# Performance work log

Hardware: AMD Instinct MI355X
Metric: run time of the kernel (lower is better)

Reference implementation:

```python
import jax, jax.numpy as jnp
import numpy as np

B, T, K = 512, 512, 128


def setup_inputs() -> dict:
    key = jax.random.key(0)
    k1, k2, k3, k4, k5 = jax.random.split(key, 5)
    emissions = jax.random.normal(k1, (B, T, K), dtype=jnp.float32)
    tags = jax.random.randint(k2, (B, T), 0, K, dtype=jnp.int64)
    mask = jnp.ones((B, T), dtype=jnp.bool_)
    # learned CRF params, init uniform(-0.1, 0.1) as in reset_parameters
    transitions = jax.random.uniform(k3, (K, K), jnp.float32, -0.1, 0.1)
    start_transitions = jax.random.uniform(k4, (K,), jnp.float32, -0.1, 0.1)
    end_transitions = jax.random.uniform(k5, (K,), jnp.float32, -0.1, 0.1)
    return {
        "emissions": emissions,
        "tags": tags,
        "mask": mask,
        "transitions": transitions,
        "start_transitions": start_transitions,
        "end_transitions": end_transitions,
    }


def _log_partition(emissions, mask, transitions, start_transitions, end_transitions):
    # emissions: [T, B, K] time-major; mask: [T, B]
    log_alpha0 = start_transitions[None, :] + emissions[0]  # [B, K]

    def step(log_alpha, inp):
        em_t, m_t = inp  # [B, K], [B]
        # inner[b, i, j] = log_alpha[b, i] + transitions[i, j] + em_t[b, j]
        inner = log_alpha[:, :, None] + transitions[None, :, :] + em_t[:, None, :]
        new = jax.nn.logsumexp(inner, axis=1)  # [B, K]
        log_alpha = jnp.where(m_t[:, None], new, log_alpha)
        return log_alpha, None

    log_alpha, _ = jax.lax.scan(step, log_alpha0, (emissions[1:], mask[1:]))
    log_alpha = log_alpha + end_transitions[None, :]
    return jax.nn.logsumexp(log_alpha, axis=1)  # [B]


def _gold_score(emissions, tags, mask, transitions, start_transitions, end_transitions):
    # time-major emissions [T, B, K], tags/mask [T, B]
    maskf = mask.astype(emissions.dtype)
    score = start_transitions[tags[0]]  # [B]
    # emission scores: gather tag emission at each step, masked
    em = jnp.take_along_axis(emissions, tags[:, :, None], axis=2)[:, :, 0]  # [T, B]
    score = score + jnp.sum(em * maskf, axis=0)
    # transition scores: transitions[tags[i], tags[i-1]] (note [to, from] order, as in source)
    trans = transitions[tags[1:], tags[:-1]]  # [T-1, B]
    score = score + jnp.sum(trans * maskf[1:], axis=0)
    last_idx = jnp.sum(mask.astype(jnp.int32), axis=0) - 1  # [B]
    last_tags = jnp.take_along_axis(tags, last_idx[None, :], axis=0)[0]  # [B]
    score = score + end_transitions[last_tags]
    return score


def reference(emissions, tags, mask, transitions, start_transitions, end_transitions):
    # batch_first=True -> transpose to time-major
    em = jnp.transpose(emissions, (1, 0, 2))  # [T, B, K]
    tg = jnp.transpose(tags, (1, 0))  # [T, B]
    mk = jnp.transpose(mask, (1, 0))  # [T, B]
    log_num = _gold_score(em, tg, mk, transitions, start_transitions, end_transitions)
    log_den = _log_partition(em, mk, transitions, start_transitions, end_transitions)
    return -jnp.mean(log_num - log_den)
```

## Files before the change

### kernel.cpp

```cpp
#include <hip/hip_runtime.h>

#define K 128
#define T 512
#define BB 512
#define PADB 20

typedef float f32x2 __attribute__((ext_vector_type(2)));
typedef float f32x4 __attribute__((ext_vector_type(4)));

#define LDS_BARRIER() asm volatile("s_waitcnt lgkmcnt(0)\ns_barrier" ::: "memory")

template <int CTRL>
__device__ __forceinline__ float qperm(float x) {
    return __int_as_float(__builtin_amdgcn_update_dpp(
        0, __float_as_int(x), CTRL, 0xF, 0xF, true));
}
#define QXOR1   0xB1
#define QXOR2   0x4E
#define HMIRROR 0x141

__global__ __launch_bounds__(512, 4) void mega_kernel(
    const float* __restrict__ em, const int* __restrict__ tags,
    const float* __restrict__ trans, const float* __restrict__ startt,
    const float* __restrict__ endt,
    float* __restrict__ log_den, float* __restrict__ log_num)
{
    const int bid  = blockIdx.x;
    const int kind = (bid ^ (bid >> 8)) & 1;
    const int b    = bid >> 1;
    const int tid  = threadIdx.x;

    __shared__ __align__(16) float stF[2][8 * PADB];
    __shared__ __align__(16) float stB[2][8 * PADB];
    __shared__ float gs[8];
    __shared__ int   iks[2];

    if (kind) {
        const int* tg = tags + (size_t)b * T;
        const float* emb = em + (size_t)b * T * K;
        int   tag = tg[tid];
        float s   = emb[(size_t)tid * K + tag];
        if (tid >= 1) s += trans[tag * K + tg[tid - 1]];
#pragma unroll
        for (int off = 32; off >= 1; off >>= 1) s += __shfl_xor(s, off);
        if ((tid & 63) == 0) gs[tid >> 6] = s;
        __syncthreads();
        if (tid == 0) {
            float tot = ((gs[0] + gs[1]) + (gs[2] + gs[3]))
                      + ((gs[4] + gs[5]) + (gs[6] + gs[7]));
            log_num[b] = tot + startt[tg[0]] + endt[tg[T - 1]];
        }
        return;
    }

    const int half = tid >> 8;
    const int h    = tid & 255;
    const int ib   = h & 7;
    const int jg   = h >> 3;
    const int own  = 4 * jg + (ib & 3);
    const bool writer = (ib < 4);
    const int wpos = (own >> 4) * PADB + (own & 15);

    f32x2 Ec[32];
    {
        const volatile float* Tv = trans;
        const int r0 = ib * 16, c0 = jg * 4;
#pragma unroll
        for (int c = 0; c < 4; ++c)
#pragma unroll
            for (int p = 0; p < 8; ++p) {
                float x0, x1;
                if (half == 0) {
                    x0 = Tv[(size_t)(r0 + 2 * p)     * K + c0 + c];
                    x1 = Tv[(size_t)(r0 + 2 * p + 1) * K + c0 + c];
                } else {
                    x0 = Tv[(size_t)(c0 + c) * K + r0 + 2 * p];
                    x1 = Tv[(size_t)(c0 + c) * K + r0 + 2 * p + 1];
                }
                Ec[c * 8 + p].x = __expf(x0);
                Ec[c * 8 + p].y = __expf(x1);
            }
    }

    const float* emb = em + (size_t)b * T * K;
    const float* emo = emb + own;

    if (tid < K) {
        const int x = tid;
        stF[0][(x >> 4) * PADB + (x & 15)] = __expf(startt[x] + emb[x]);
    } else if (tid >= 256 && tid < 256 + K) {
        const int x = tid - 256;
        stB[0][(x >> 4) * PADB + (x & 15)] =
            __expf(endt[x] + emb[(size_t)(T - 1) * K + x]);
    }

    float ex = 0.f, r1 = 0.f, r2 = 0.f, r3 = 0.f;
    if (writer) {
        if (half == 0) {
            ex = __expf(emo[(size_t)1 * K]);
            r1 = emo[(size_t)2 * K]; r2 = emo[(size_t)3 * K]; r3 = emo[(size_t)4 * K];
        } else {
            ex = __expf(emo[(size_t)510 * K]);
            r1 = emo[(size_t)509 * K]; r2 = emo[(size_t)508 * K]; r3 = emo[(size_t)507 * K];
        }
    }

    LDS_BARRIER();

    int   ksum = 0;
    float ycur = 0.f;

    for (int it = 0; it < 256; ++it) {
        const bool active = (half == 0) || (it >= 1);
        const float* RB = (half == 0) ? stF[it & 1]       : stB[(it - 1) & 1];
        float*       WB = (half == 0) ? stF[(it + 1) & 1] : stB[it & 1];

        if (active) {
            float u0 = RB[0];
            const float* rb = RB + ib * PADB;

            f32x4 q0 = *reinterpret_cast<const f32x4*>(rb + 0);
            f32x4 q1 = *reinterpret_cast<const f32x4*>(rb + 4);
            f32x4 q2 = *reinterpret_cast<const f32x4*>(rb + 8);
            f32x4 q3 = *reinterpret_cast<const f32x4*>(rb + 12);
            f32x2 e0; e0.x = q0.x; e0.y = q0.y;
            f32x2 e1; e1.x = q0.z; e1.y = q0.w;
            f32x2 e2; e2.x = q1.x; e2.y = q1.y;
            f32x2 e3; e3.x = q1.z; e3.y = q1.w;
            f32x2 e4; e4.x = q2.x; e4.y = q2.y;
            f32x2 e5; e5.x = q2.z; e5.y = q2.w;
            f32x2 e6; e6.x = q3.x; e6.y = q3.y;
            f32x2 e7; e7.x = q3.z; e7.y = q3.w;

            f32x2 a0 = e0 * Ec[ 0]; a0 += e1 * Ec[ 1]; a0 += e2 * Ec[ 2]; a0 += e3 * Ec[ 3];
            a0 += e4 * Ec[ 4]; a0 += e5 * Ec[ 5]; a0 += e6 * Ec[ 6]; a0 += e7 * Ec[ 7];
            f32x2 a1 = e0 * Ec[ 8]; a1 += e1 * Ec[ 9]; a1 += e2 * Ec[10]; a1 += e3 * Ec[11];
            a1 += e4 * Ec[12]; a1 += e5 * Ec[13]; a1 += e6 * Ec[14]; a1 += e7 * Ec[15];
            f32x2 a2 = e0 * Ec[16]; a2 += e1 * Ec[17]; a2 += e2 * Ec[18]; a2 += e3 * Ec[19];
            a2 += e4 * Ec[20]; a2 += e5 * Ec[21]; a2 += e6 * Ec[22]; a2 += e7 * Ec[23];
            f32x2 a3 = e0 * Ec[24]; a3 += e1 * Ec[25]; a3 += e2 * Ec[26]; a3 += e3 * Ec[27];
            a3 += e4 * Ec[28]; a3 += e5 * Ec[29]; a3 += e6 * Ec[30]; a3 += e7 * Ec[31];

            f32x2 c01, c23;
            c01.x = a0.x + a0.y;  c01.y = a1.x + a1.y;
            c23.x = a2.x + a2.y;  c23.y = a3.x + a3.y;

            f32x2 tv;
            tv.x = qperm<QXOR1>(c01.x);   tv.y = qperm<QXOR1>(c01.y);   c01 += tv;
            tv.x = qperm<QXOR1>(c23.x);   tv.y = qperm<QXOR1>(c23.y);   c23 += tv;
            tv.x = qperm<QXOR2>(c01.x);   tv.y = qperm<QXOR2>(c01.y);   c01 += tv;
            tv.x = qperm<QXOR2>(c23.x);   tv.y = qperm<QXOR2>(c23.y);   c23 += tv;
            tv.x = qperm<HMIRROR>(c01.x); tv.y = qperm<HMIRROR>(c01.y); c01 += tv;
            tv.x = qperm<HMIRROR>(c23.x); tv.y = qperm<HMIRROR>(c23.y); c23 += tv;

            int   k  = (int)((__float_as_uint(u0) >> 23) & 255u) - 126;
            float sc = __uint_as_float((unsigned)(127 - k) << 23);
            ksum += k;

            float ya   = (ib & 1) ? c01.y : c01.x;
            float yb   = (ib & 1) ? c23.y : c23.x;
            float yown = (ib & 2) ? yb : ya;
            float exu  = (half == 1 && it == 255) ? 1.0f : ex;
            ycur = yown * (exu * sc);

            if (writer) {
                WB[wpos] = ycur;
                ex = __expf(r1);
                r1 = r2; r2 = r3;
                if (half == 0) {
                    int tn = it + 5; if (tn > T - 1) tn = T - 1;
                    r3 = emo[(size_t)tn * K];
                } else {
                    int tn = 507 - it; if (tn < 0) tn = 0;
                    r3 = emo[(size_t)tn * K];
                }
            }
        }

        LDS_BARRIER();
    }

    if (tid == 0)   iks[0] = ksum;
    if (tid == 256) iks[1] = ksum;
    __syncthreads();
    if (tid < 64) {
        const int x = tid, x2 = tid + 64;
        const int p1 = (x  >> 4) * PADB + (x  & 15);
        const int p2 = (x2 >> 4) * PADB + (x2 & 15);
        float v = stF[0][p1] * stB[1][p1] + stF[0][p2] * stB[1][p2];
#pragma unroll
        for (int off = 32; off >= 1; off >>= 1) v += __shfl_xor(v, off);
        if (tid == 0)
            log_den[b] = (float)((double)(iks[0] + iks[1]) * 0.6931471805599453)
                       + __logf(v);
    }
}

__global__ __launch_bounds__(512) void reduce_kernel(
    const float* __restrict__ log_num, const float* __restrict__ log_den,
    float* __restrict__ out)
{
    __shared__ float buf[BB];
    const int i = threadIdx.x;
    buf[i] = log_num[i] - log_den[i];
    __syncthreads();
#pragma unroll
    for (int sft = 256; sft >= 1; sft >>= 1) {
        if (i < sft) buf[i] += buf[i + sft];
        __syncthreads();
    }
    if (i == 0) out[0] = -buf[0] / (float)BB;
}

extern "C" void kernel_launch(void* const* d_in, const int* in_sizes, int n_in,
                              void* d_out, int out_size, void* d_ws, size_t ws_size,
                              hipStream_t stream)
{
    const float* em     = (const float*)d_in[0];
    const int*   tags   = (const int*)d_in[1];
    const float* trans  = (const float*)d_in[3];
    const float* startt = (const float*)d_in[4];
    const float* endt   = (const float*)d_in[5];

    float* ws      = (float*)d_ws;
    float* log_den = ws;
    float* log_num = ws + BB;
    float* out     = (float*)d_out;

    mega_kernel<<<2 * BB, 512, 0, stream>>>(em, tags, trans, startt, endt,
                                            log_den, log_num);
    reduce_kernel<<<1, BB, 0, stream>>>(log_num, log_den, out);
}
```

Measured before the change: 217.9 us.

## Halve block size so each thread computes eight output columns instead of four

Shrinks the CRF forward/backward block from 512 to 256 threads. Each thread now holds 8 columns of exp(transitions) in registers (64 float2) and produces 8 outputs, so every lane writes one state and the redundant half-wave of non-writer reducers is gone. The gold-score blocks handle two timesteps per thread. This cuts per-block thread count and barrier participants but doubles register pressure per thread, which may limit occupancy and lengthen the serial per-step chain.

```diff
diff --git a/kernel.cpp b/kernel.cpp
--- a/kernel.cpp
+++ b/kernel.cpp
@@ -19,7 +19,7 @@
 #define QXOR2   0x4E
 #define HMIRROR 0x141
 
-__global__ __launch_bounds__(512, 4) void mega_kernel(
+__global__ __launch_bounds__(256, 2) void mega_kernel(
     const float* __restrict__ em, const int* __restrict__ tags,
     const float* __restrict__ trans, const float* __restrict__ startt,
     const float* __restrict__ endt,
@@ -32,41 +32,43 @@
 
     __shared__ __align__(16) float stF[2][8 * PADB];
     __shared__ __align__(16) float stB[2][8 * PADB];
-    __shared__ float gs[8];
+    __shared__ float gs[4];
     __shared__ int   iks[2];
 
     if (kind) {
         const int* tg = tags + (size_t)b * T;
         const float* emb = em + (size_t)b * T * K;
-        int   tag = tg[tid];
-        float s   = emb[(size_t)tid * K + tag];
-        if (tid >= 1) s += trans[tag * K + tg[tid - 1]];
+        float s = 0.f;
+#pragma unroll
+        for (int tt = 0; tt < 2; ++tt) {
+            const int t = tid + tt * 256;
+            int tag = tg[t];
+            s += emb[(size_t)t * K + tag];
+            if (t >= 1) s += trans[tag * K + tg[t - 1]];
+        }
 #pragma unroll
         for (int off = 32; off >= 1; off >>= 1) s += __shfl_xor(s, off);
         if ((tid & 63) == 0) gs[tid >> 6] = s;
         __syncthreads();
-        if (tid == 0) {
-            float tot = ((gs[0] + gs[1]) + (gs[2] + gs[3]))
-                      + ((gs[4] + gs[5]) + (gs[6] + gs[7]));
-            log_num[b] = tot + startt[tg[0]] + endt[tg[T - 1]];
-        }
+        if (tid == 0)
+            log_num[b] = (gs[0] + gs[1]) + (gs[2] + gs[3])
+                       + startt[tg[0]] + endt[tg[T - 1]];
         return;
     }
 
-    const int half = tid >> 8;
-    const int h    = tid & 255;
+    const int half = tid >> 7;
+    const int h    = tid & 127;
     const int ib   = h & 7;
     const int jg   = h >> 3;
-    const int own  = 4 * jg + (ib & 3);
-    const bool writer = (ib < 4);
+    const int own  = 8 * jg + ib;
     const int wpos = (own >> 4) * PADB + (own & 15);
 
-    f32x2 Ec[32];
+    f32x2 Ec[64];
     {
         const volatile float* Tv = trans;
-        const int r0 = ib * 16, c0 = jg * 4;
-#pragma unroll
-        for (int c = 0; c < 4; ++c)
+        const int r0 = ib * 16, c0 = jg * 8;
+#pragma unroll
+        for (int c = 0; c < 8; ++c)
 #pragma unroll
             for (int p = 0; p < 8; ++p) {
                 float x0, x1;
@@ -88,27 +90,24 @@
     if (tid < K) {
         const int x = tid;
         stF[0][(x >> 4) * PADB + (x & 15)] = __expf(startt[x] + emb[x]);
-    } else if (tid >= 256 && tid < 256 + K) {
-        const int x = tid - 256;
+    } else {
+        const int x = tid - 128;
         stB[0][(x >> 4) * PADB + (x & 15)] =
             __expf(endt[x] + emb[(size_t)(T - 1) * K + x]);
     }
 
-    float ex = 0.f, r1 = 0.f, r2 = 0.f, r3 = 0.f;
-    if (writer) {
-        if (half == 0) {
-            ex = __expf(emo[(size_t)1 * K]);
-            r1 = emo[(size_t)2 * K]; r2 = emo[(size_t)3 * K]; r3 = emo[(size_t)4 * K];
-        } else {
-            ex = __expf(emo[(size_t)510 * K]);
-            r1 = emo[(size_t)509 * K]; r2 = emo[(size_t)508 * K]; r3 = emo[(size_t)507 * K];
-        }
+    float ex, r1, r2, r3;
+    if (half == 0) {
+        ex = __expf(emo[(size_t)1 * K]);
+        r1 = emo[(size_t)2 * K]; r2 = emo[(size_t)3 * K]; r3 = emo[(size_t)4 * K];
+    } else {
+        ex = __expf(emo[(size_t)510 * K]);
+        r1 = emo[(size_t)509 * K]; r2 = emo[(size_t)508 * K]; r3 = emo[(size_t)507 * K];
     }
 
     LDS_BARRIER();
 
     int   ksum = 0;
-    float ycur = 0.f;
 
     for (int it = 0; it < 256; ++it) {
         const bool active = (half == 0) || (it >= 1);
@@ -132,48 +131,52 @@
             f32x2 e6; e6.x = q3.x; e6.y = q3.y;
             f32x2 e7; e7.x = q3.z; e7.y = q3.w;
 
-            f32x2 a0 = e0 * Ec[ 0]; a0 += e1 * Ec[ 1]; a0 += e2 * Ec[ 2]; a0 += e3 * Ec[ 3];
-            a0 += e4 * Ec[ 4]; a0 += e5 * Ec[ 5]; a0 += e6 * Ec[ 6]; a0 += e7 * Ec[ 7];
-            f32x2 a1 = e0 * Ec[ 8]; a1 += e1 * Ec[ 9]; a1 += e2 * Ec[10]; a1 += e3 * Ec[11];
-            a1 += e4 * Ec[12]; a1 += e5 * Ec[13]; a1 += e6 * Ec[14]; a1 += e7 * Ec[15];
-            f32x2 a2 = e0 * Ec[16]; a2 += e1 * Ec[17]; a2 += e2 * Ec[18]; a2 += e3 * Ec[19];
-            a2 += e4 * Ec[20]; a2 += e5 * Ec[21]; a2 += e6 * Ec[22]; a2 += e7 * Ec[23];
-            f32x2 a3 = e0 * Ec[24]; a3 += e1 * Ec[25]; a3 += e2 * Ec[26]; a3 += e3 * Ec[27];
-            a3 += e4 * Ec[28]; a3 += e5 * Ec[29]; a3 += e6 * Ec[30]; a3 += e7 * Ec[31];
-
-            f32x2 c01, c23;
+            f32x2 a0, a1, a2, a3, a4, a5, a6, a7;
+#define COLA(A, CBASE)                                                        \
+            A  = e0 * Ec[(CBASE)*8 + 0]; A += e1 * Ec[(CBASE)*8 + 1];          \
+            A += e2 * Ec[(CBASE)*8 + 2]; A += e3 * Ec[(CBASE)*8 + 3];          \
+            A += e4 * Ec[(CBASE)*8 + 4]; A += e5 * Ec[(CBASE)*8 + 5];          \
+            A += e6 * Ec[(CBASE)*8 + 6]; A += e7 * Ec[(CBASE)*8 + 7];
+            COLA(a0, 0) COLA(a1, 1) COLA(a2, 2) COLA(a3, 3)
+            COLA(a4, 4) COLA(a5, 5) COLA(a6, 6) COLA(a7, 7)
+#undef COLA
+
+            f32x2 c01, c23, c45, c67;
             c01.x = a0.x + a0.y;  c01.y = a1.x + a1.y;
             c23.x = a2.x + a2.y;  c23.y = a3.x + a3.y;
+            c45.x = a4.x + a4.y;  c45.y = a5.x + a5.y;
+            c67.x = a6.x + a6.y;  c67.y = a7.x + a7.y;
 
             f32x2 tv;
-            tv.x = qperm<QXOR1>(c01.x);   tv.y = qperm<QXOR1>(c01.y);   c01 += tv;
-            tv.x = qperm<QXOR1>(c23.x);   tv.y = qperm<QXOR1>(c23.y);   c23 += tv;
-            tv.x = qperm<QXOR2>(c01.x);   tv.y = qperm<QXOR2>(c01.y);   c01 += tv;
-            tv.x = qperm<QXOR2>(c23.x);   tv.y = qperm<QXOR2>(c23.y);   c23 += tv;
-            tv.x = qperm<HMIRROR>(c01.x); tv.y = qperm<HMIRROR>(c01.y); c01 += tv;
-            tv.x = qperm<HMIRROR>(c23.x); tv.y = qperm<HMIRROR>(c23.y); c23 += tv;
+#define RED(LVL)                                                              \
+            tv.x = qperm<LVL>(c01.x); tv.y = qperm<LVL>(c01.y); c01 += tv;     \
+            tv.x = qperm<LVL>(c23.x); tv.y = qperm<LVL>(c23.y); c23 += tv;     \
+            tv.x = qperm<LVL>(c45.x); tv.y = qperm<LVL>(c45.y); c45 += tv;     \
+            tv.x = qperm<LVL>(c67.x); tv.y = qperm<LVL>(c67.y); c67 += tv;
+            RED(QXOR1)
+            RED(QXOR2)
+            RED(HMIRROR)
+#undef RED
 
             int   k  = (int)((__float_as_uint(u0) >> 23) & 255u) - 126;
             float sc = __uint_as_float((unsigned)(127 - k) << 23);
             ksum += k;
 
-            float ya   = (ib & 1) ? c01.y : c01.x;
-            float yb   = (ib & 1) ? c23.y : c23.x;
-            float yown = (ib & 2) ? yb : ya;
+            f32x2 s1 = (ib & 2) ? c23 : c01;
+            f32x2 s2 = (ib & 2) ? c67 : c45;
+            f32x2 s3 = (ib & 4) ? s2  : s1;
+            float yown = (ib & 1) ? s3.y : s3.x;
             float exu  = (half == 1 && it == 255) ? 1.0f : ex;
-            ycur = yown * (exu * sc);
-
-            if (writer) {
-                WB[wpos] = ycur;
-                ex = __expf(r1);
-                r1 = r2; r2 = r3;
-                if (half == 0) {
-                    int tn = it + 5; if (tn > T - 1) tn = T - 1;
-                    r3 = emo[(size_t)tn * K];
-                } else {
-                    int tn = 507 - it; if (tn < 0) tn = 0;
-                    r3 = emo[(size_t)tn * K];
-                }
+            WB[wpos] = yown * (exu * sc);
+
+            ex = __expf(r1);
+            r1 = r2; r2 = r3;
+            if (half == 0) {
+                int tn = it + 5; if (tn > T - 1) tn = T - 1;
+                r3 = emo[(size_t)tn * K];
+            } else {
+                int tn = 507 - it; if (tn < 0) tn = 0;
+                r3 = emo[(size_t)tn * K];
             }
         }
 
@@ -181,7 +184,7 @@
     }
 
     if (tid == 0)   iks[0] = ksum;
-    if (tid == 256) iks[1] = ksum;
+    if (tid == 128) iks[1] = ksum;
     __syncthreads();
     if (tid < 64) {
         const int x = tid, x2 = tid + 64;
@@ -227,7 +230,7 @@
     float* log_num = ws + BB;
     float* out     = (float*)d_out;
 
-    mega_kernel<<<2 * BB, 512, 0, stream>>>(em, tags, trans, startt, endt,
+    mega_kernel<<<2 * BB, 256, 0, stream>>>(em, tags, trans, startt, endt,
                                             log_den, log_num);
     reduce_kernel<<<1, BB, 0, stream>>>(log_num, log_den, out);
 }
```

New measurement: 295.4 us. +35.6%, slower.

## Split forward/backward CRF recursions into separate 256-thread blocks with combine kernel

Applied to the files above, without the earlier changes.

The forward and backward halves of each sequence's partition recursion, which previously shared one 512-thread block, now run in independent 256-thread blocks. A third block per sequence computes the gold score. The final dot product of the forward and backward state vectors moves to a new combine kernel that reads them from workspace. This removes the barrier coupling between the two halves and lets more, smaller blocks run per CU, at the cost of an extra kernel launch and a global round trip for the state vectors.

```diff
diff --git a/kernel.cpp b/kernel.cpp
--- a/kernel.cpp
+++ b/kernel.cpp
@@ -19,47 +19,50 @@
 #define QXOR2   0x4E
 #define HMIRROR 0x141
 
-__global__ __launch_bounds__(512, 4) void mega_kernel(
+__global__ __launch_bounds__(256, 6) void mega_kernel(
     const float* __restrict__ em, const int* __restrict__ tags,
     const float* __restrict__ trans, const float* __restrict__ startt,
     const float* __restrict__ endt,
-    float* __restrict__ log_den, float* __restrict__ log_num)
+    float* __restrict__ aout, float* __restrict__ bout,
+    float* __restrict__ ksout, float* __restrict__ log_num)
 {
     const int bid  = blockIdx.x;
-    const int kind = (bid ^ (bid >> 8)) & 1;
-    const int b    = bid >> 1;
+    const int kind = bid % 3;
+    const int b    = bid / 3;
     const int tid  = threadIdx.x;
 
-    __shared__ __align__(16) float stF[2][8 * PADB];
-    __shared__ __align__(16) float stB[2][8 * PADB];
-    __shared__ float gs[8];
-    __shared__ int   iks[2];
-
-    if (kind) {
+    __shared__ __align__(16) float st[2][8 * PADB];
+    __shared__ float gs[4];
+
+    const float* emb = em + (size_t)b * T * K;
+
+    if (kind == 2) {
         const int* tg = tags + (size_t)b * T;
-        const float* emb = em + (size_t)b * T * K;
-        int   tag = tg[tid];
-        float s   = emb[(size_t)tid * K + tag];
-        if (tid >= 1) s += trans[tag * K + tg[tid - 1]];
+        float s = 0.f;
+#pragma unroll
+        for (int tt = 0; tt < 2; ++tt) {
+            const int t = tid + tt * 256;
+            int tag = tg[t];
+            s += emb[(size_t)t * K + tag];
+            if (t >= 1) s += trans[tag * K + tg[t - 1]];
+        }
 #pragma unroll
         for (int off = 32; off >= 1; off >>= 1) s += __shfl_xor(s, off);
         if ((tid & 63) == 0) gs[tid >> 6] = s;
         __syncthreads();
-        if (tid == 0) {
-            float tot = ((gs[0] + gs[1]) + (gs[2] + gs[3]))
-                      + ((gs[4] + gs[5]) + (gs[6] + gs[7]));
-            log_num[b] = tot + startt[tg[0]] + endt[tg[T - 1]];
-        }
+        if (tid == 0)
+            log_num[b] = (gs[0] + gs[1]) + (gs[2] + gs[3])
+                       + startt[tg[0]] + endt[tg[T - 1]];
         return;
     }
 
-    const int half = tid >> 8;
-    const int h    = tid & 255;
-    const int ib   = h & 7;
-    const int jg   = h >> 3;
+    const int half = kind;
+    const int ib   = tid & 7;
+    const int jg   = tid >> 3;
     const int own  = 4 * jg + (ib & 3);
     const bool writer = (ib < 4);
     const int wpos = (own >> 4) * PADB + (own & 15);
+    const int NIT  = (half == 0) ? 256 : 255;
 
     f32x2 Ec[32];
     {
@@ -82,16 +85,14 @@
             }
     }
 
-    const float* emb = em + (size_t)b * T * K;
     const float* emo = emb + own;
 
     if (tid < K) {
-        const int x = tid;
-        stF[0][(x >> 4) * PADB + (x & 15)] = __expf(startt[x] + emb[x]);
-    } else if (tid >= 256 && tid < 256 + K) {
-        const int x = tid - 256;
-        stB[0][(x >> 4) * PADB + (x & 15)] =
-            __expf(endt[x] + emb[(size_t)(T - 1) * K + x]);
+        const int p = (tid >> 4) * PADB + (tid & 15);
+        if (half == 0)
+            st[0][p] = __expf(startt[tid] + emb[tid]);
+        else
+            st[0][p] = __expf(endt[tid] + emb[(size_t)(T - 1) * K + tid]);
     }
 
     float ex = 0.f, r1 = 0.f, r2 = 0.f, r3 = 0.f;
@@ -107,92 +108,96 @@
 
     LDS_BARRIER();
 
-    int   ksum = 0;
-    float ycur = 0.f;
-
-    for (int it = 0; it < 256; ++it) {
-        const bool active = (half == 0) || (it >= 1);
-        const float* RB = (half == 0) ? stF[it & 1]       : stB[(it - 1) & 1];
-        float*       WB = (half == 0) ? stF[(it + 1) & 1] : stB[it & 1];
-
-        if (active) {
-            float u0 = RB[0];
-            const float* rb = RB + ib * PADB;
-
-            f32x4 q0 = *reinterpret_cast<const f32x4*>(rb + 0);
-            f32x4 q1 = *reinterpret_cast<const f32x4*>(rb + 4);
-            f32x4 q2 = *reinterpret_cast<const f32x4*>(rb + 8);
-            f32x4 q3 = *reinterpret_cast<const f32x4*>(rb + 12);
-            f32x2 e0; e0.x = q0.x; e0.y = q0.y;
-            f32x2 e1; e1.x = q0.z; e1.y = q0.w;
-            f32x2 e2; e2.x = q1.x; e2.y = q1.y;
-            f32x2 e3; e3.x = q1.z; e3.y = q1.w;
-            f32x2 e4; e4.x = q2.x; e4.y = q2.y;
-            f32x2 e5; e5.x = q2.z; e5.y = q2.w;
-            f32x2 e6; e6.x = q3.x; e6.y = q3.y;
-            f32x2 e7; e7.x = q3.z; e7.y = q3.w;
-
-            f32x2 a0 = e0 * Ec[ 0]; a0 += e1 * Ec[ 1]; a0 += e2 * Ec[ 2]; a0 += e3 * Ec[ 3];
-            a0 += e4 * Ec[ 4]; a0 += e5 * Ec[ 5]; a0 += e6 * Ec[ 6]; a0 += e7 * Ec[ 7];
-            f32x2 a1 = e0 * Ec[ 8]; a1 += e1 * Ec[ 9]; a1 += e2 * Ec[10]; a1 += e3 * Ec[11];
-            a1 += e4 * Ec[12]; a1 += e5 * Ec[13]; a1 += e6 * Ec[14]; a1 += e7 * Ec[15];
-            f32x2 a2 = e0 * Ec[16]; a2 += e1 * Ec[17]; a2 += e2 * Ec[18]; a2 += e3 * Ec[19];
-            a2 += e4 * Ec[20]; a2 += e5 * Ec[21]; a2 += e6 * Ec[22]; a2 += e7 * Ec[23];
-            f32x2 a3 = e0 * Ec[24]; a3 += e1 * Ec[25]; a3 += e2 * Ec[26]; a3 += e3 * Ec[27];
-            a3 += e4 * Ec[28]; a3 += e5 * Ec[29]; a3 += e6 * Ec[30]; a3 += e7 * Ec[31];
-
-            f32x2 c01, c23;
-            c01.x = a0.x + a0.y;  c01.y = a1.x + a1.y;
-            c23.x = a2.x + a2.y;  c23.y = a3.x + a3.y;
-
-            f32x2 tv;
-            tv.x = qperm<QXOR1>(c01.x);   tv.y = qperm<QXOR1>(c01.y);   c01 += tv;
-            tv.x = qperm<QXOR1>(c23.x);   tv.y = qperm<QXOR1>(c23.y);   c23 += tv;
-            tv.x = qperm<QXOR2>(c01.x);   tv.y = qperm<QXOR2>(c01.y);   c01 += tv;
-            tv.x = qperm<QXOR2>(c23.x);   tv.y = qperm<QXOR2>(c23.y);   c23 += tv;
-            tv.x = qperm<HMIRROR>(c01.x); tv.y = qperm<HMIRROR>(c01.y); c01 += tv;
-            tv.x = qperm<HMIRROR>(c23.x); tv.y = qperm<HMIRROR>(c23.y); c23 += tv;
-
-            int   k  = (int)((__float_as_uint(u0) >> 23) & 255u) - 126;
-            float sc = __uint_as_float((unsigned)(127 - k) << 23);
-            ksum += k;
-
-            float ya   = (ib & 1) ? c01.y : c01.x;
-            float yb   = (ib & 1) ? c23.y : c23.x;
-            float yown = (ib & 2) ? yb : ya;
-            float exu  = (half == 1 && it == 255) ? 1.0f : ex;
-            ycur = yown * (exu * sc);
-
-            if (writer) {
-                WB[wpos] = ycur;
-                ex = __expf(r1);
-                r1 = r2; r2 = r3;
-                if (half == 0) {
-                    int tn = it + 5; if (tn > T - 1) tn = T - 1;
-                    r3 = emo[(size_t)tn * K];
-                } else {
-                    int tn = 507 - it; if (tn < 0) tn = 0;
-                    r3 = emo[(size_t)tn * K];
-                }
+    int ksum = 0;
+
+    for (int it = 0; it < NIT; ++it) {
+        const float* RB = st[it & 1];
+        float*       WB = st[(it + 1) & 1];
+
+        float u0 = RB[0];
+        const float* rb = RB + ib * PADB;
+
+        f32x4 q0 = *reinterpret_cast<const f32x4*>(rb + 0);
+        f32x4 q1 = *reinterpret_cast<const f32x4*>(rb + 4);
+        f32x4 q2 = *reinterpret_cast<const f32x4*>(rb + 8);
+        f32x4 q3 = *reinterpret_cast<const f32x4*>(rb + 12);
+        f32x2 e0; e0.x = q0.x; e0.y = q0.y;
+        f32x2 e1; e1.x = q0.z; e1.y = q0.w;
+        f32x2 e2; e2.x = q1.x; e2.y = q1.y;
+        f32x2 e3; e3.x = q1.z; e3.y = q1.w;
+        f32x2 e4; e4.x = q2.x; e4.y = q2.y;
+        f32x2 e5; e5.x = q2.z; e5.y = q2.w;
+        f32x2 e6; e6.x = q3.x; e6.y = q3.y;
+        f32x2 e7; e7.x = q3.z; e7.y = q3.w;
+
+        f32x2 a0 = e0 * Ec[ 0]; a0 += e1 * Ec[ 1]; a0 += e2 * Ec[ 2]; a0 += e3 * Ec[ 3];
+        a0 += e4 * Ec[ 4]; a0 += e5 * Ec[ 5]; a0 += e6 * Ec[ 6]; a0 += e7 * Ec[ 7];
+        f32x2 a1 = e0 * Ec[ 8]; a1 += e1 * Ec[ 9]; a1 += e2 * Ec[10]; a1 += e3 * Ec[11];
+        a1 += e4 * Ec[12]; a1 += e5 * Ec[13]; a1 += e6 * Ec[14]; a1 += e7 * Ec[15];
+        f32x2 a2 = e0 * Ec[16]; a2 += e1 * Ec[17]; a2 += e2 * Ec[18]; a2 += e3 * Ec[19];
+        a2 += e4 * Ec[20]; a2 += e5 * Ec[21]; a2 += e6 * Ec[22]; a2 += e7 * Ec[23];
+        f32x2 a3 = e0 * Ec[24]; a3 += e1 * Ec[25]; a3 += e2 * Ec[26]; a3 += e3 * Ec[27];
+        a3 += e4 * Ec[28]; a3 += e5 * Ec[29]; a3 += e6 * Ec[30]; a3 += e7 * Ec[31];
+
+        f32x2 c01, c23;
+        c01.x = a0.x + a0.y;  c01.y = a1.x + a1.y;
+        c23.x = a2.x + a2.y;  c23.y = a3.x + a3.y;
+
+        f32x2 tv;
+        tv.x = qperm<QXOR1>(c01.x);   tv.y = qperm<QXOR1>(c01.y);   c01 += tv;
+        tv.x = qperm<QXOR1>(c23.x);   tv.y = qperm<QXOR1>(c23.y);   c23 += tv;
+        tv.x = qperm<QXOR2>(c01.x);   tv.y = qperm<QXOR2>(c01.y);   c01 += tv;
+        tv.x = qperm<QXOR2>(c23.x);   tv.y = qperm<QXOR2>(c23.y);   c23 += tv;
+        tv.x = qperm<HMIRROR>(c01.x); tv.y = qperm<HMIRROR>(c01.y); c01 += tv;
+        tv.x = qperm<HMIRROR>(c23.x); tv.y = qperm<HMIRROR>(c23.y); c23 += tv;
+
+        int   k  = (int)((__float_as_uint(u0) >> 23) & 255u) - 126;
+        float sc = __uint_as_float((unsigned)(127 - k) << 23);
+        ksum += k;
+
+        float ya   = (ib & 1) ? c01.y : c01.x;
+        float yb   = (ib & 1) ? c23.y : c23.x;
+        float yown = (ib & 2) ? yb : ya;
+        float exu  = (half == 1 && it == 254) ? 1.0f : ex;
+
+        if (writer) {
+            WB[wpos] = yown * (exu * sc);
+            ex = __expf(r1);
+            r1 = r2; r2 = r3;
+            if (half == 0) {
+                int tn = it + 5; if (tn > T - 1) tn = T - 1;
+                r3 = emo[(size_t)tn * K];
+            } else {
+                int tn = 506 - it; if (tn < 0) tn = 0;
+                r3 = emo[(size_t)tn * K];
             }
         }
 
         LDS_BARRIER();
     }
 
-    if (tid == 0)   iks[0] = ksum;
-    if (tid == 256) iks[1] = ksum;
-    __syncthreads();
-    if (tid < 64) {
-        const int x = tid, x2 = tid + 64;
-        const int p1 = (x  >> 4) * PADB + (x  & 15);
-        const int p2 = (x2 >> 4) * PADB + (x2 & 15);
-        float v = stF[0][p1] * stB[1][p1] + stF[0][p2] * stB[1][p2];
-#pragma unroll
-        for (int off = 32; off >= 1; off >>= 1) v += __shfl_xor(v, off);
-        if (tid == 0)
-            log_den[b] = (float)((double)(iks[0] + iks[1]) * 0.6931471805599453)
-                       + __logf(v);
+    float* outv = (half == 0) ? (aout + (size_t)b * K) : (bout + (size_t)b * K);
+    const float* S = (half == 0) ? st[0] : st[1];
+    if (tid < K)
+        outv[tid] = S[(tid >> 4) * PADB + (tid & 15)];
+    if (tid == 0)
+        ksout[2 * b + half] = (float)ksum;
+}
+
+__global__ __launch_bounds__(64) void combine_kernel(
+    const float* __restrict__ aout, const float* __restrict__ bout,
+    const float* __restrict__ ksout, float* __restrict__ log_den)
+{
+    const int b = blockIdx.x;
+    const int l = threadIdx.x;
+    f32x2 av = *reinterpret_cast<const f32x2*>(aout + (size_t)b * K + 2 * l);
+    f32x2 bv = *reinterpret_cast<const f32x2*>(bout + (size_t)b * K + 2 * l);
+    float v = av.x * bv.x + av.y * bv.y;
+#pragma unroll
+    for (int off = 32; off >= 1; off >>= 1) v += __shfl_xor(v, off);
+    if (l == 0) {
+        double ks = (double)ksout[2 * b] + (double)ksout[2 * b + 1];
+        log_den[b] = (float)(ks * 0.6931471805599453) + __logf(v);
     }
 }
 
@@ -223,11 +228,15 @@
     const float* endt   = (const float*)d_in[5];
 
     float* ws      = (float*)d_ws;
-    float* log_den = ws;
-    float* log_num = ws + BB;
+    float* aout    = ws;
+    float* bout    = aout + (size_t)BB * K;
+    float* ksout   = bout + (size_t)BB * K;
+    float* log_num = ksout + 2 * BB;
+    float* log_den = log_num + BB;
     float* out     = (float*)d_out;
 
-    mega_kernel<<<2 * BB, 512, 0, stream>>>(em, tags, trans, startt, endt,
-                                            log_den, log_num);
+    mega_kernel<<<3 * BB, 256, 0, stream>>>(em, tags, trans, startt, endt,
+                                            aout, bout, ksout, log_num);
+    combine_kernel<<<BB, 64, 0, stream>>>(aout, bout, ksout, log_den);
     reduce_kernel<<<1, BB, 0, stream>>>(log_num, log_den, out);
 }
```

Result: slower. 360.5 us (+65.4%).
